# Kernel optimization log

Hardware: AMD Instinct MI355X
Metric: run time of the kernel (lower is better)

## Reference

```python
import jax, jax.numpy as jnp
import numpy as np

N, K, C, S = 40000, 16, 128, 8  # points, neighbors, channels, share_planes
EPS = 1e-5


def _bn(x, g, b, m, v):
    # eval-mode BatchNorm1d over the channel (last) axis
    return (x - m) * (g * jax.lax.rsqrt(v + EPS)) + b


def _forward(xyz, feats, Wq, bq, Wk, bk, Wv, bv, Wp1, bp1, p_gamma, p_beta, p_mean, p_var,
             Wp2, bp2, w_gamma, w_beta, w_mean, w_var, Ww1, bw1, w1_gamma, w1_beta,
             w1_mean, w1_var, Ww2, bw2, nei_ind):
    x = feats[0]          # (N, C)
    pos = xyz[0]          # (N, 3)
    idx = nei_ind[0]      # (N, K)

    q = x @ Wq + bq                      # (N, C)
    kf = (x @ Wk + bk)[idx]              # (N, K, C) neighbor gather
    vf = (x @ Wv + bv)[idx]              # (N, K, C)

    d = pos[idx] - pos[:, None, :]       # (N, K, 3) relative positions
    # linear_p: Linear_BN(3,3) -> ReLU -> Linear(3, C)
    p = jax.nn.relu(_bn(d @ Wp1 + bp1, p_gamma, p_beta, p_mean, p_var)) @ Wp2 + bp2  # (N, K, C)

    # mid_planes == out_planes, so the view(...,1,mid).sum(2) is an identity reshape
    w = kf - q[:, None, :] + p           # (N, K, C)
    w = _bn(w, w_gamma, w_beta, w_mean, w_var)  # bn_w over channels
    # linear_w: ReLU -> Linear_BN(C, C//S) -> ReLU -> Linear(C//S, C//S)
    w = jax.nn.relu(_bn(jax.nn.relu(w) @ Ww1 + bw1, w1_gamma, w1_beta, w1_mean, w1_var)) @ Ww2 + bw2  # (N, K, C//S)
    w = jax.nn.softmax(w, axis=1)        # softmax over K neighbors

    # grouped-channel weighted sum over neighbors
    agg = ((vf + p).reshape(N, K, S, C // S) * w[:, :, None, :]).sum(axis=1).reshape(N, C)

    # shortcut is Identity (in_planes == out_planes); broadcast over batch dim like torch
    return jax.nn.leaky_relu(agg[None, :, :] + feats, negative_slope=0.1)  # (1, N, C)


def setup_inputs() -> dict:
    key = jax.random.key(0)
    ks = jax.random.split(key, 16)
    f32 = jnp.float32

    def w(k, shape, scale):
        return jax.random.normal(k, shape, dtype=f32) * scale

    return {
        "xyz": jax.random.uniform(ks[0], (1, N, 3), dtype=f32),
        "feats": jax.random.normal(ks[1], (1, N, C), dtype=f32),
        "nei_ind": jax.random.randint(ks[2], (1, N, K), 0, N, dtype=jnp.int32),
        "Wq": w(ks[3], (C, C), C ** -0.5), "bq": jnp.zeros((C,), f32),
        "Wk": w(ks[4], (C, C), C ** -0.5), "bk": jnp.zeros((C,), f32),
        "Wv": w(ks[5], (C, C), C ** -0.5), "bv": jnp.zeros((C,), f32),
        "Wp1": w(ks[6], (3, 3), 0.5), "bp1": jnp.zeros((3,), f32),
        "p_gamma": jnp.ones((3,), f32), "p_beta": jnp.zeros((3,), f32),
        "p_mean": w(ks[7], (3,), 0.1), "p_var": jnp.ones((3,), f32),
        "Wp2": w(ks[8], (3, C), 0.5), "bp2": jnp.zeros((C,), f32),
        "w_gamma": jnp.ones((C,), f32), "w_beta": jnp.zeros((C,), f32),
        "w_mean": w(ks[9], (C,), 0.1), "w_var": jnp.ones((C,), f32),
        "Ww1": w(ks[10], (C, C // S), C ** -0.5), "bw1": jnp.zeros((C // S,), f32),
        "w1_gamma": jnp.ones((C // S,), f32), "w1_beta": jnp.zeros((C // S,), f32),
        "w1_mean": w(ks[11], (C // S,), 0.1), "w1_var": jnp.ones((C // S,), f32),
        "Ww2": w(ks[12], (C // S, C // S), (C // S) ** -0.5), "bw2": jnp.zeros((C // S,), f32),
    }


def reference(xyz, feats, nei_ind, Wq, bq, Wk, bk, Wv, bv, Wp1, bp1, p_gamma, p_beta,
              p_mean, p_var, Wp2, bp2, w_gamma, w_beta, w_mean, w_var, Ww1, bw1,
              w1_gamma, w1_beta, w1_mean, w1_var, Ww2, bw2):
    return _forward(xyz, feats, Wq, bq, Wk, bk, Wv, bv, Wp1, bp1, p_gamma, p_beta,
                    p_mean, p_var, Wp2, bp2, w_gamma, w_beta, w_mean, w_var, Ww1, bw1,
                    w1_gamma, w1_beta, w1_mean, w1_var, Ww2, bw2, nei_ind)
```

## Files before the change

kernel.cpp:

```cpp
#include <hip/hip_runtime.h>
#include <stdint.h>

#define N_PTS 40000
#define KNBR  16
#define CH    128
#define EPSV  1e-5f

typedef __attribute__((ext_vector_type(4))) float f32x4;
typedef __attribute__((ext_vector_type(8))) short bf16x8;

__device__ __forceinline__ float bf2f(ushort u) {
    union { uint32_t i; float f; } x; x.i = ((uint32_t)u) << 16; return x.f;
}
__device__ __forceinline__ float bflo(uint32_t u) {
    union { uint32_t i; float f; } x; x.i = u << 16; return x.f;
}
__device__ __forceinline__ float bfhi(uint32_t u) {
    union { uint32_t i; float f; } x; x.i = u & 0xffff0000u; return x.f;
}
__device__ __forceinline__ ushort f2bf(float f) {
    union { float f; uint32_t i; } x; x.f = f;
    uint32_t i = x.i;
    i += 0x7fffu + ((i >> 16) & 1u);
    return (ushort)(i >> 16);
}

#if __has_builtin(__builtin_amdgcn_cvt_pk_bf16_f32)
typedef __bf16 bf16x2v __attribute__((ext_vector_type(2)));
__device__ __forceinline__ uint32_t pack2(float a, float b) {
    union { bf16x2v v; uint32_t u; } x;
    x.v = __builtin_amdgcn_cvt_pk_bf16_f32(a, b);
    return x.u;
}
#else
__device__ __forceinline__ uint32_t pack2(float a, float b) {
    return (uint32_t)f2bf(a) | ((uint32_t)f2bf(b) << 16);
}
#endif

template <bool BF> struct IO;
template <> struct IO<true> {
    static __device__ __forceinline__ float  ld (const void* p, int i) { return bf2f(((const ushort*)p)[i]); }
    static __device__ __forceinline__ float2 ld2(const void* p, int i) { const uint32_t u = ((const uint32_t*)p)[i]; return make_float2(bflo(u), bfhi(u)); }
    static __device__ __forceinline__ ushort ldbf(const void* p, int i) { return ((const ushort*)p)[i]; }
    static __device__ __forceinline__ void   st2(void* p, int i, float a, float b) { ((uint32_t*)p)[i] = pack2(a, b); }
};
template <> struct IO<false> {
    static __device__ __forceinline__ float  ld (const void* p, int i) { return ((const float*)p)[i]; }
    static __device__ __forceinline__ float2 ld2(const void* p, int i) { return ((const float2*)p)[i]; }
    static __device__ __forceinline__ ushort ldbf(const void* p, int i) { return f2bf(((const float*)p)[i]); }
    static __device__ __forceinline__ void   st2(void* p, int i, float a, float b) { ((float2*)p)[i] = make_float2(a, b); }
};

__device__ __forceinline__ bool detect_bf16(const void* w_var) {
    return (*(const uint32_t*)w_var & 0xffffu) != 0u;
}

#define PROJ_BLOCKS 1250
template <bool BF>
__device__ void proj_body(
    const void* feats,
    const void* Wq, const void* bq, const void* Wk, const void* bk,
    const void* Wv, const void* bv,
    uint32_t* qws, uint4* kvws)
{
    const int l    = threadIdx.x & 63;
    const int w    = threadIdx.x >> 6;
    const int t    = l & 15;
    const int quad = l >> 4;
    const int cq   = w;

    const void* Wsrc[3] = { Wq, Wk, Wv };
    const void* bsrc[3] = { bq, bk, bv };

    bf16x8 afrag[3][4];
    float  bias[3][4];
    #pragma unroll
    for (int m = 0; m < 3; ++m) {
        #pragma unroll
        for (int s = 0; s < 4; ++s)
            #pragma unroll
            for (int j = 0; j < 8; ++j) {
                const int k = s * 32 + quad * 8 + j;
                afrag[m][s][j] = (short)IO<BF>::ldbf(Wsrc[m], k * CH + cq * 16 + t);
            }
        #pragma unroll
        for (int r = 0; r < 4; ++r)
            bias[m][r] = IO<BF>::ld(bsrc[m], cq * 16 + quad * 4 + r);
    }

    #pragma unroll
    for (int n = 0; n < 2; ++n) {
        const int tt = blockIdx.x + PROJ_BLOCKS * n;
        const int p0 = tt * 16;
        bf16x8 bfr[4];
        if (BF) {
            const ushort* xp = (const ushort*)feats + (p0 + t) * CH + quad * 8;
            #pragma unroll
            for (int s = 0; s < 4; ++s)
                bfr[s] = *(const bf16x8*)(xp + s * 32);
        } else {
            const float* xp = (const float*)feats + (p0 + t) * CH + quad * 8;
            #pragma unroll
            for (int s = 0; s < 4; ++s) {
                const float4 a = *(const float4*)(xp + s * 32);
                const float4 b = *(const float4*)(xp + s * 32 + 4);
                bfr[s][0] = (short)f2bf(a.x); bfr[s][1] = (short)f2bf(a.y);
                bfr[s][2] = (short)f2bf(a.z); bfr[s][3] = (short)f2bf(a.w);
                bfr[s][4] = (short)f2bf(b.x); bfr[s][5] = (short)f2bf(b.y);
                bfr[s][6] = (short)f2bf(b.z); bfr[s][7] = (short)f2bf(b.w);
            }
        }
        f32x4 acc[3];
        #pragma unroll
        for (int m = 0; m < 3; ++m) {
            acc[m] = f32x4{ bias[m][0], bias[m][1], bias[m][2], bias[m][3] };
            #pragma unroll
            for (int s = 0; s < 4; ++s)
                acc[m] = __builtin_amdgcn_mfma_f32_16x16x32_bf16(afrag[m][s], bfr[s], acc[m], 0, 0, 0);
        }
        const int p = p0 + t;
        const int m16 = cq * 4 + quad;
        uint2 qo;
        qo.x = pack2(acc[0][0], acc[0][1]);
        qo.y = pack2(acc[0][2], acc[0][3]);
        ((uint2*)qws)[p * 32 + m16] = qo;
        uint4 kv;
        kv.x = pack2(acc[1][0], acc[1][1]);
        kv.y = pack2(acc[2][0], acc[2][1]);
        kv.z = pack2(acc[1][2], acc[1][3]);
        kv.w = pack2(acc[2][2], acc[2][3]);
        kvws[p * 32 + m16] = kv;
    }
}

__global__ __launch_bounds__(512) void proj_kernel(
    const void* feats, const void* Wq, const void* bq, const void* Wk,
    const void* bk, const void* Wv, const void* bv, const void* w_var_probe,
    uint32_t* qws, uint4* kvws)
{
    if (detect_bf16(w_var_probe))
        proj_body<true >(feats, Wq, bq, Wk, bk, Wv, bv, qws, kvws);
    else
        proj_body<false>(feats, Wq, bq, Wk, bk, Wv, bv, qws, kvws);
}

template <bool BF>
__device__ void attn_body(
    const void* xyz, const void* feats, const int* __restrict__ nei,
    const uint32_t* __restrict__ qws, const uint2* __restrict__ kvws,
    const void* Wp1, const void* bp1, const void* p_gamma, const void* p_beta,
    const void* p_mean, const void* p_var, const void* Wp2, const void* bp2,
    const void* w_gamma, const void* w_beta, const void* w_mean, const void* w_var,
    const void* Ww1, const void* bw1, const void* w1_gamma, const void* w1_beta,
    const void* w1_mean, const void* w1_var, const void* Ww2, const void* bw2,
    void* out, ushort* wbuf, ushort* ubuf, float* wsm, float* hlds,
    int i0, int l)
{
    const int t = l & 15;
    const int quad = l >> 4;

    float A1[3][3], C1[3];
    #pragma unroll
    for (int b = 0; b < 3; ++b) {
        const float sb = IO<BF>::ld(p_gamma, b) * rsqrtf(IO<BF>::ld(p_var, b) + EPSV);
        C1[b] = (IO<BF>::ld(bp1, b) - IO<BF>::ld(p_mean, b)) * sb + IO<BF>::ld(p_beta, b);
        #pragma unroll
        for (int a = 0; a < 3; ++a) A1[a][b] = IO<BF>::ld(Wp1, a * 3 + b) * sb;
    }

    const float2 vg = IO<BF>::ld2(w_gamma, l);
    const float2 vb = IO<BF>::ld2(w_beta, l);
    const float2 vm = IO<BF>::ld2(w_mean, l);
    const float2 vv = IO<BF>::ld2(w_var, l);
    const float scw0 = vg.x * rsqrtf(vv.x + EPSV);
    const float scw1 = vg.y * rsqrtf(vv.y + EPSV);
    const float shw0 = vb.x - vm.x * scw0;
    const float shw1 = vb.y - vm.y * scw1;

    float wp2c[3][2];
    #pragma unroll
    for (int r = 0; r < 3; ++r) {
        const float2 u = IO<BF>::ld2(Wp2, r * 64 + l);
        wp2c[r][0] = u.x; wp2c[r][1] = u.y;
    }
    const float2 vbp2 = IO<BF>::ld2(bp2, l);
    const float bp20 = vbp2.x, bp21 = vbp2.y;

    bf16x8 bfrag1[4];
    #pragma unroll
    for (int s = 0; s < 4; ++s)
        #pragma unroll
        for (int kk = 0; kk < 8; ++kk) {
            const int k = s * 32 + quad * 8 + kk;
            bfrag1[s][kk] = (short)IO<BF>::ldbf(Ww1, k * 16 + t);
        }
    bf16x8 bfrag2;
    #pragma unroll
    for (int kk = 0; kk < 8; ++kk) {
        const int k = quad * 8 + kk;
        bfrag2[kk] = (quad < 2) ? (short)IO<BF>::ldbf(Ww2, k * 16 + t) : (short)0;
    }

    const float s1t  = IO<BF>::ld(w1_gamma, t) * rsqrtf(IO<BF>::ld(w1_var, t) + EPSV);
    const float sh1t = IO<BF>::ld(w1_beta, t) - IO<BF>::ld(w1_mean, t) * s1t;
    const float bw1t = IO<BF>::ld(bw1, t);
    const float bw2t = IO<BF>::ld(bw2, t);

    #pragma unroll 1
    for (int pp = 0; pp < 4; ++pp) {
        const int i = i0 + pp;

        const uint32_t uq = qws[i * 64 + l];
        const float qs0 = shw0 - bflo(uq) * scw0;
        const float qs1 = shw1 - bfhi(uq) * scw1;

        const float pix = IO<BF>::ld(xyz, i * 3 + 0);
        const float piy = IO<BF>::ld(xyz, i * 3 + 1);
        const float piz = IO<BF>::ld(xyz, i * 3 + 2);

        const int vnj = nei[i * KNBR + t];
        const float ndx = IO<BF>::ld(xyz, vnj * 3 + 0) - pix;
        const float ndy = IO<BF>::ld(xyz, vnj * 3 + 1) - piy;
        const float ndz = IO<BF>::ld(xyz, vnj * 3 + 2) - piz;
        const float hh0 = fmaxf(0.f, ndx * A1[0][0] + ndy * A1[1][0] + ndz * A1[2][0] + C1[0]);
        const float hh1 = fmaxf(0.f, ndx * A1[0][1] + ndy * A1[1][1] + ndz * A1[2][1] + C1[1]);
        const float hh2 = fmaxf(0.f, ndx * A1[0][2] + ndy * A1[1][2] + ndz * A1[2][2] + C1[2]);
        if (quad == 0)
            *(float4*)&hlds[t * 4] = make_float4(hh0, hh1, hh2, 0.f);

        int njs[KNBR];
        #pragma unroll
        for (int j = 0; j < KNBR; ++j) njs[j] = nei[i * KNBR + j];
        uint2 kv[KNBR];
        #pragma unroll
        for (int j = 0; j < KNBR; ++j) kv[j] = kvws[njs[j] * 64 + l];

        float vfp0[KNBR], vfp1[KNBR];
        #pragma unroll
        for (int j = 0; j < KNBR; ++j) {
            const float4 h = *(const float4*)&hlds[j * 4];
            const float p0 = h.x * wp2c[0][0] + h.y * wp2c[1][0] + h.z * wp2c[2][0] + bp20;
            const float p1 = h.x * wp2c[0][1] + h.y * wp2c[1][1] + h.z * wp2c[2][1] + bp21;
            vfp0[j] = bflo(kv[j].y) + p0;
            vfp1[j] = bfhi(kv[j].y) + p1;
            const float w0 = fmaxf(0.f, fmaf(bflo(kv[j].x) + p0, scw0, qs0));
            const float w1 = fmaxf(0.f, fmaf(bfhi(kv[j].x) + p1, scw1, qs1));
            ((uint32_t*)wbuf)[j * 68 + l] = pack2(w0, w1);
        }

        f32x4 acc1 = { bw1t, bw1t, bw1t, bw1t };
        const ushort* arow = &wbuf[t * 136 + quad * 8];
        #pragma unroll
        for (int s = 0; s < 4; ++s) {
            const bf16x8 afrag = *(const bf16x8*)(arow + s * 32);
            acc1 = __builtin_amdgcn_mfma_f32_16x16x32_bf16(afrag, bfrag1[s], acc1, 0, 0, 0);
        }
        #pragma unroll
        for (int r = 0; r < 4; ++r) {
            const float u = fmaxf(0.f, acc1[r] * s1t + sh1t);
            ubuf[(quad * 4 + r) * 24 + t] = f2bf(u);
        }

        f32x4 acc2 = { bw2t, bw2t, bw2t, bw2t };
        bf16x8 afrag2;
        if (quad < 2) {
            afrag2 = *(const bf16x8*)(&ubuf[t * 24 + quad * 8]);
        } else {
            #pragma unroll
            for (int kk = 0; kk < 8; ++kk) afrag2[kk] = 0;
        }
        acc2 = __builtin_amdgcn_mfma_f32_16x16x32_bf16(afrag2, bfrag2, acc2, 0, 0, 0);

        float z0 = acc2[0], z1 = acc2[1], z2 = acc2[2], z3 = acc2[3];
        float mx = fmaxf(fmaxf(z0, z1), fmaxf(z2, z3));
        mx = fmaxf(mx, __shfl_xor(mx, 16));
        mx = fmaxf(mx, __shfl_xor(mx, 32));
        const float e0 = __expf(z0 - mx), e1 = __expf(z1 - mx);
        const float e2 = __expf(z2 - mx), e3 = __expf(z3 - mx);
        float ssum = e0 + e1 + e2 + e3;
        ssum += __shfl_xor(ssum, 16);
        ssum += __shfl_xor(ssum, 32);
        const float inv = 1.0f / ssum;
        wsm[(quad * 4 + 0) * 18 + t] = e0 * inv;
        wsm[(quad * 4 + 1) * 18 + t] = e1 * inv;
        wsm[(quad * 4 + 2) * 18 + t] = e2 * inv;
        wsm[(quad * 4 + 3) * 18 + t] = e3 * inv;

        const int t0 = (2 * l) & 15;
        float agg0 = 0.f, agg1 = 0.f;
        #pragma unroll
        for (int j = 0; j < KNBR; ++j) {
            const float2 wp = *(const float2*)&wsm[j * 18 + t0];
            agg0 = fmaf(vfp0[j], wp.x, agg0);
            agg1 = fmaf(vfp1[j], wp.y, agg1);
        }
        const float2 xf = IO<BF>::ld2(feats, i * 64 + l);
        float o0 = agg0 + xf.x;
        float o1 = agg1 + xf.y;
        o0 = o0 > 0.f ? o0 : 0.1f * o0;
        o1 = o1 > 0.f ? o1 : 0.1f * o1;
        IO<BF>::st2(out, i * 64 + l, o0, o1);
    }
}

__global__ __launch_bounds__(256) void attn_kernel(
    const void* xyz, const void* feats, const int* __restrict__ nei,
    const uint32_t* __restrict__ qws, const uint2* __restrict__ kvws,
    const void* Wp1, const void* bp1, const void* p_gamma, const void* p_beta,
    const void* p_mean, const void* p_var, const void* Wp2, const void* bp2,
    const void* w_gamma, const void* w_beta, const void* w_mean, const void* w_var,
    const void* Ww1, const void* bw1, const void* w1_gamma, const void* w1_beta,
    const void* w1_mean, const void* w1_var, const void* Ww2, const void* bw2,
    void* out)
{
    __shared__ ushort wbuf[4][16 * 136];
    __shared__ ushort ubuf[4][16 * 24];
    __shared__ float  wsm [4][16 * 18];
    __shared__ float  hlds[4][16 * 4];

    const int wave = threadIdx.x >> 6;
    const int l    = threadIdx.x & 63;
    const int i0   = blockIdx.x * 16 + wave * 4;

    if (detect_bf16(w_var))
        attn_body<true >(xyz, feats, nei, qws, kvws, Wp1, bp1, p_gamma, p_beta,
                         p_mean, p_var, Wp2, bp2, w_gamma, w_beta, w_mean, w_var,
                         Ww1, bw1, w1_gamma, w1_beta, w1_mean, w1_var, Ww2, bw2,
                         out, wbuf[wave], ubuf[wave], wsm[wave], hlds[wave], i0, l);
    else
        attn_body<false>(xyz, feats, nei, qws, kvws, Wp1, bp1, p_gamma, p_beta,
                         p_mean, p_var, Wp2, bp2, w_gamma, w_beta, w_mean, w_var,
                         Ww1, bw1, w1_gamma, w1_beta, w1_mean, w1_var, Ww2, bw2,
                         out, wbuf[wave], ubuf[wave], wsm[wave], hlds[wave], i0, l);
}

extern "C" void kernel_launch(void* const* d_in, const int* in_sizes, int n_in,
                              void* d_out, int out_size, void* d_ws, size_t ws_size,
                              hipStream_t stream) {
    const void* xyz     = d_in[0];
    const void* feats   = d_in[1];
    const int*  nei     = (const int*)d_in[2];
    const void* Wq      = d_in[3];
    const void* bq      = d_in[4];
    const void* Wk      = d_in[5];
    const void* bk      = d_in[6];
    const void* Wv      = d_in[7];
    const void* bv      = d_in[8];
    const void* Wp1     = d_in[9];
    const void* bp1     = d_in[10];
    const void* p_gamma = d_in[11];
    const void* p_beta  = d_in[12];
    const void* p_mean  = d_in[13];
    const void* p_var   = d_in[14];
    const void* Wp2     = d_in[15];
    const void* bp2     = d_in[16];
    const void* w_gamma = d_in[17];
    const void* w_beta  = d_in[18];
    const void* w_mean  = d_in[19];
    const void* w_var   = d_in[20];
    const void* Ww1     = d_in[21];
    const void* bw1     = d_in[22];
    const void* w1_gamma= d_in[23];
    const void* w1_beta = d_in[24];
    const void* w1_mean = d_in[25];
    const void* w1_var  = d_in[26];
    const void* Ww2     = d_in[27];
    const void* bw2     = d_in[28];

    uint32_t* qws  = (uint32_t*)d_ws;
    uint4*    kvws = (uint4*)(qws + (size_t)N_PTS * 64);

    proj_kernel<<<PROJ_BLOCKS, 512, 0, stream>>>(feats, Wq, bq, Wk, bk, Wv, bv, w_var,
                                                 qws, kvws);
    attn_kernel<<<N_PTS / 16, 256, 0, stream>>>(xyz, feats, nei, qws, (const uint2*)kvws,
                                          Wp1, bp1, p_gamma, p_beta, p_mean, p_var,
                                          Wp2, bp2, w_gamma, w_beta, w_mean, w_var,
                                          Ww1, bw1, w1_gamma, w1_beta, w1_mean, w1_var,
                                          Ww2, bw2, d_out);
}
```

Baseline: 223.1 us.

## Software-pipeline neighbor K/V gathers across points with double-buffered registers

```diff
diff --git a/kernel.cpp b/kernel.cpp
--- a/kernel.cpp
+++ b/kernel.cpp
@@ -207,10 +207,8 @@
     const float bw1t = IO<BF>::ld(bw1, t);
     const float bw2t = IO<BF>::ld(bw2, t);
 
-    #pragma unroll 1
-    for (int pp = 0; pp < 4; ++pp) {
-        const int i = i0 + pp;
-
+    auto point = [&](int i, const int (&njs)[KNBR], uint2 (&kv)[KNBR],
+                     bool pf, int inext, int (&njsn)[KNBR], uint2 (&kvn)[KNBR]) {
         const uint32_t uq = qws[i * 64 + l];
         const float qs0 = shw0 - bflo(uq) * scw0;
         const float qs1 = shw1 - bfhi(uq) * scw1;
@@ -219,7 +217,7 @@
         const float piy = IO<BF>::ld(xyz, i * 3 + 1);
         const float piz = IO<BF>::ld(xyz, i * 3 + 2);
 
-        const int vnj = nei[i * KNBR + t];
+        const int vnj = njs[t];
         const float ndx = IO<BF>::ld(xyz, vnj * 3 + 0) - pix;
         const float ndy = IO<BF>::ld(xyz, vnj * 3 + 1) - piy;
         const float ndz = IO<BF>::ld(xyz, vnj * 3 + 2) - piz;
@@ -229,24 +227,23 @@
         if (quad == 0)
             *(float4*)&hlds[t * 4] = make_float4(hh0, hh1, hh2, 0.f);
 
-        int njs[KNBR];
-        #pragma unroll
-        for (int j = 0; j < KNBR; ++j) njs[j] = nei[i * KNBR + j];
-        uint2 kv[KNBR];
-        #pragma unroll
-        for (int j = 0; j < KNBR; ++j) kv[j] = kvws[njs[j] * 64 + l];
-
-        float vfp0[KNBR], vfp1[KNBR];
+        uint32_t vfp[KNBR];
         #pragma unroll
         for (int j = 0; j < KNBR; ++j) {
             const float4 h = *(const float4*)&hlds[j * 4];
             const float p0 = h.x * wp2c[0][0] + h.y * wp2c[1][0] + h.z * wp2c[2][0] + bp20;
             const float p1 = h.x * wp2c[0][1] + h.y * wp2c[1][1] + h.z * wp2c[2][1] + bp21;
-            vfp0[j] = bflo(kv[j].y) + p0;
-            vfp1[j] = bfhi(kv[j].y) + p1;
+            vfp[j] = pack2(bflo(kv[j].y) + p0, bfhi(kv[j].y) + p1);
             const float w0 = fmaxf(0.f, fmaf(bflo(kv[j].x) + p0, scw0, qs0));
             const float w1 = fmaxf(0.f, fmaf(bfhi(kv[j].x) + p1, scw1, qs1));
             ((uint32_t*)wbuf)[j * 68 + l] = pack2(w0, w1);
+        }
+
+        if (pf) {
+            #pragma unroll
+            for (int j = 0; j < KNBR; ++j) njsn[j] = nei[inext * KNBR + j];
+            #pragma unroll
+            for (int j = 0; j < KNBR; ++j) kvn[j] = kvws[njsn[j] * 64 + l];
         }
 
         f32x4 acc1 = { bw1t, bw1t, bw1t, bw1t };
@@ -292,16 +289,28 @@
         #pragma unroll
         for (int j = 0; j < KNBR; ++j) {
             const float2 wp = *(const float2*)&wsm[j * 18 + t0];
-            agg0 = fmaf(vfp0[j], wp.x, agg0);
-            agg1 = fmaf(vfp1[j], wp.y, agg1);
+            agg0 = fmaf(bflo(vfp[j]), wp.x, agg0);
+            agg1 = fmaf(bfhi(vfp[j]), wp.y, agg1);
         }
         const float2 xf = IO<BF>::ld2(feats, i * 64 + l);
         float o0 = agg0 + xf.x;
         float o1 = agg1 + xf.y;
-        o0 = o0 > 0.f ? o0 : 0.1f * o0;
-        o1 = o1 > 0.f ? o1 : 0.1f * o1;
+        o0 = fmaxf(o0, 0.1f * o0);
+        o1 = fmaxf(o1, 0.1f * o1);
         IO<BF>::st2(out, i * 64 + l, o0, o1);
-    }
+    };
+
+    int  njsA[KNBR], njsB[KNBR];
+    uint2 kvA[KNBR], kvB[KNBR];
+    #pragma unroll
+    for (int j = 0; j < KNBR; ++j) njsA[j] = nei[i0 * KNBR + j];
+    #pragma unroll
+    for (int j = 0; j < KNBR; ++j) kvA[j] = kvws[njsA[j] * 64 + l];
+
+    point(i0 + 0, njsA, kvA, true,  i0 + 1, njsB, kvB);
+    point(i0 + 1, njsB, kvB, true,  i0 + 2, njsA, kvA);
+    point(i0 + 2, njsA, kvA, true,  i0 + 3, njsB, kvB);
+    point(i0 + 3, njsB, kvB, false, i0 + 3, njsA, kvA);
 }
 
 __global__ __launch_bounds__(256) void attn_kernel(
```

After: 240.5 us. +7.8%, slower.
